# Performance work log

Hardware: AMD Instinct MI355X
Metric: run time of the kernel (lower is better)

The kernel has to match this reference:

```python
import jax, jax.numpy as jnp
import numpy as np

N = 16384


def setup_inputs() -> dict:
    key = jax.random.key(0)
    k1, k2 = jax.random.split(key)
    y_pred = jax.random.normal(k1, (N,), dtype=jnp.float32)
    y_true = jax.random.randint(k2, (N,), 0, 2, dtype=jnp.int32)
    return {"y_pred": y_pred, "y_true": y_true}


def reference(y_pred, y_true):
    # sigmoid scores
    s = jax.nn.sigmoid(y_pred)  # [N]
    pos = (y_true == 1)
    neg = (y_true == 0)
    P = jnp.sum(pos).astype(s.dtype)
    Q = jnp.sum(neg).astype(s.dtype)
    # pairwise hinge: relu(1 - (s_p - s_n)) over all (pos, neg) pairs
    diff = s[:, None] - s[None, :]                  # [N, N]
    hinge = jnp.maximum(1.0 - diff, 0.0)            # [N, N]
    mask = pos[:, None] & neg[None, :]               # [N, N] bool
    total = jnp.sum(jnp.where(mask, hinge, 0.0))
    denom = P * Q
    # original returns 0.0 if either class is empty
    return jnp.where(denom > 0, total / jnp.maximum(denom, 1.0), 0.0)
```

## Files before the change

kernel.cpp:

```cpp
#include <hip/hip_runtime.h>
#include <math.h>


__global__ __launch_bounds__(1024)
void auroc_reduce(const float* __restrict__ yp,
                  const int*   __restrict__ yt,
                  float*       __restrict__ out,
                  int n)
{
    const int tid = threadIdx.x;

    float sp = 0.0f, sn = 0.0f;
    int   cp = 0,    cq = 0;

    const int n4 = n >> 2;
    const float4* __restrict__ yp4 = (const float4*)yp;
    const int4*   __restrict__ yt4 = (const int4*)yt;
    for (int i = tid; i < n4; i += 1024) {
        float4 x = yp4[i];
        int4   t = yt4[i];
        float s;
        s = 1.0f / (1.0f + __expf(-x.x)); if (t.x == 1) { sp += s; ++cp; } else if (t.x == 0) { sn += s; ++cq; }
        s = 1.0f / (1.0f + __expf(-x.y)); if (t.y == 1) { sp += s; ++cp; } else if (t.y == 0) { sn += s; ++cq; }
        s = 1.0f / (1.0f + __expf(-x.z)); if (t.z == 1) { sp += s; ++cp; } else if (t.z == 0) { sn += s; ++cq; }
        s = 1.0f / (1.0f + __expf(-x.w)); if (t.w == 1) { sp += s; ++cp; } else if (t.w == 0) { sn += s; ++cq; }
    }
    for (int i = (n4 << 2) + tid; i < n; i += 1024) {
        float s = 1.0f / (1.0f + __expf(-yp[i]));
        int t = yt[i];
        if (t == 1) { sp += s; ++cp; } else if (t == 0) { sn += s; ++cq; }
    }

    float fp = (float)cp, fq = (float)cq;

    #pragma unroll
    for (int off = 32; off > 0; off >>= 1) {
        sp += __shfl_down(sp, off);
        sn += __shfl_down(sn, off);
        fp += __shfl_down(fp, off);
        fq += __shfl_down(fq, off);
    }

    __shared__ float red[16][4];
    const int wave = tid >> 6;
    const int lane = tid & 63;
    if (lane == 0) {
        red[wave][0] = sp;
        red[wave][1] = sn;
        red[wave][2] = fp;
        red[wave][3] = fq;
    }
    __syncthreads();

    if (tid == 0) {
        float tsp = 0.0f, tsn = 0.0f, tp = 0.0f, tq = 0.0f;
        #pragma unroll
        for (int w = 0; w < 16; ++w) {
            tsp += red[w][0];
            tsn += red[w][1];
            tp  += red[w][2];
            tq  += red[w][3];
        }
        float denom = tp * tq;
        float total = tp * tq - tq * tsp + tp * tsn;
        out[0] = (denom > 0.0f) ? (total / fmaxf(denom, 1.0f)) : 0.0f;
    }
}

extern "C" void kernel_launch(void* const* d_in, const int* in_sizes, int n_in,
                              void* d_out, int out_size, void* d_ws, size_t ws_size,
                              hipStream_t stream) {
    const float* y_pred = (const float*)d_in[0];
    const int*   y_true = (const int*)d_in[1];
    float* out = (float*)d_out;
    const int n = in_sizes[0];

    auroc_reduce<<<1, 1024, 0, stream>>>(y_pred, y_true, out, n);
}
```

Measured before the change: 9.696 us.

## Split reduction across multiple blocks with fixed-point atomics and last-block finalize

```diff
diff --git a/kernel.cpp b/kernel.cpp
--- a/kernel.cpp
+++ b/kernel.cpp
@@ -2,33 +2,42 @@
 #include <math.h>
 
 
-__global__ __launch_bounds__(1024)
-void auroc_reduce(const float* __restrict__ yp,
-                  const int*   __restrict__ yt,
-                  float*       __restrict__ out,
-                  int n)
+#define TPB   256
+#define NBLK  16
+#define SCALE 68719476736.0
+
+__global__ void auroc_init(unsigned long long* __restrict__ acc) {
+    if (threadIdx.x < 8) acc[threadIdx.x] = 0ull;
+}
+
+__global__ __launch_bounds__(TPB)
+void auroc_main(const float* __restrict__ yp,
+                const int*   __restrict__ yt,
+                float*       __restrict__ out,
+                unsigned long long* __restrict__ acc,
+                int n)
 {
     const int tid = threadIdx.x;
+    const int n4  = n >> 2;
 
     float sp = 0.0f, sn = 0.0f;
     int   cp = 0,    cq = 0;
 
-    const int n4 = n >> 2;
-    const float4* __restrict__ yp4 = (const float4*)yp;
-    const int4*   __restrict__ yt4 = (const int4*)yt;
-    for (int i = tid; i < n4; i += 1024) {
-        float4 x = yp4[i];
-        int4   t = yt4[i];
+    for (int i = blockIdx.x * TPB + tid; i < n4; i += gridDim.x * TPB) {
+        float4 x = ((const float4*)yp)[i];
+        int4   t = ((const int4*)yt)[i];
         float s;
         s = 1.0f / (1.0f + __expf(-x.x)); if (t.x == 1) { sp += s; ++cp; } else if (t.x == 0) { sn += s; ++cq; }
         s = 1.0f / (1.0f + __expf(-x.y)); if (t.y == 1) { sp += s; ++cp; } else if (t.y == 0) { sn += s; ++cq; }
         s = 1.0f / (1.0f + __expf(-x.z)); if (t.z == 1) { sp += s; ++cp; } else if (t.z == 0) { sn += s; ++cq; }
         s = 1.0f / (1.0f + __expf(-x.w)); if (t.w == 1) { sp += s; ++cp; } else if (t.w == 0) { sn += s; ++cq; }
     }
-    for (int i = (n4 << 2) + tid; i < n; i += 1024) {
-        float s = 1.0f / (1.0f + __expf(-yp[i]));
-        int t = yt[i];
-        if (t == 1) { sp += s; ++cp; } else if (t == 0) { sn += s; ++cq; }
+    if (blockIdx.x == 0) {
+        for (int i = (n4 << 2) + tid; i < n; i += TPB) {
+            float s = 1.0f / (1.0f + __expf(-yp[i]));
+            int t = yt[i];
+            if (t == 1) { sp += s; ++cp; } else if (t == 0) { sn += s; ++cq; }
+        }
     }
 
     float fp = (float)cp, fq = (float)cq;
@@ -41,29 +50,33 @@
         fq += __shfl_down(fq, off);
     }
 
-    __shared__ float red[16][4];
-    const int wave = tid >> 6;
-    const int lane = tid & 63;
-    if (lane == 0) {
-        red[wave][0] = sp;
-        red[wave][1] = sn;
-        red[wave][2] = fp;
-        red[wave][3] = fq;
-    }
+    __shared__ float red[4][4];
+    const int wave = tid >> 6, lane = tid & 63;
+    if (lane == 0) { red[wave][0]=sp; red[wave][1]=sn; red[wave][2]=fp; red[wave][3]=fq; }
     __syncthreads();
 
     if (tid == 0) {
-        float tsp = 0.0f, tsn = 0.0f, tp = 0.0f, tq = 0.0f;
+        float bsp=0, bsn=0, bfp=0, bfq=0;
         #pragma unroll
-        for (int w = 0; w < 16; ++w) {
-            tsp += red[w][0];
-            tsn += red[w][1];
-            tp  += red[w][2];
-            tq  += red[w][3];
+        for (int w = 0; w < 4; ++w) { bsp+=red[w][0]; bsn+=red[w][1]; bfp+=red[w][2]; bfq+=red[w][3]; }
+
+        atomicAdd(&acc[0], (unsigned long long)(bfp + 0.5f));
+        atomicAdd(&acc[1], (unsigned long long)(bfq + 0.5f));
+        atomicAdd(&acc[2], (unsigned long long)((double)bsp * SCALE));
+        atomicAdd(&acc[3], (unsigned long long)((double)bsn * SCALE));
+        __threadfence();
+        unsigned long long old = atomicAdd(&acc[4], 1ull);
+        if (old == (unsigned long long)(gridDim.x - 1)) {
+            unsigned long long P_  = atomicAdd(&acc[0], 0ull);
+            unsigned long long Q_  = atomicAdd(&acc[1], 0ull);
+            unsigned long long SpF = atomicAdd(&acc[2], 0ull);
+            unsigned long long SnF = atomicAdd(&acc[3], 0ull);
+            double P = (double)P_, Q = (double)Q_;
+            double Sp = (double)SpF * (1.0 / SCALE);
+            double Sn = (double)SnF * (1.0 / SCALE);
+            double res = (P > 0.0 && Q > 0.0) ? (1.0 - Sp / P + Sn / Q) : 0.0;
+            out[0] = (float)res;
         }
-        float denom = tp * tq;
-        float total = tp * tq - tq * tsp + tp * tsn;
-        out[0] = (denom > 0.0f) ? (total / fmaxf(denom, 1.0f)) : 0.0f;
     }
 }
 
@@ -73,7 +86,9 @@
     const float* y_pred = (const float*)d_in[0];
     const int*   y_true = (const int*)d_in[1];
     float* out = (float*)d_out;
+    unsigned long long* acc = (unsigned long long*)d_ws;
     const int n = in_sizes[0];
 
-    auroc_reduce<<<1, 1024, 0, stream>>>(y_pred, y_true, out, n);
+    auroc_init<<<1, 64, 0, stream>>>(acc);
+    auroc_main<<<NBLK, TPB, 0, stream>>>(y_pred, y_true, out, acc, n);
 }
```

New measurement: 19.68 us. 2.03x slower.
